# Kernel optimization log

Hardware: AMD Instinct MI355X
Metric: run time of the kernel (lower is better)

## Reference

```python
import jax, jax.numpy as jnp
import numpy as np

COULOMB_CONSTANT = -1.0
EV = 1.602e-19
MAX_ELEMENT = 100
N_ATOMS = 4096
HIDDEN = 16
EMB_ROWS = MAX_ELEMENT * (MAX_ELEMENT + 1) // 2  # 5050


def setup_inputs() -> dict:
    key = jax.random.key(0)
    ks = jax.random.split(key, 8)
    coordinates = jax.random.normal(ks[0], (N_ATOMS, 3), dtype=jnp.float32) * 5.0
    atom_ix = jax.random.randint(ks[1], (N_ATOMS,), 0, MAX_ELEMENT)
    charges = jax.random.normal(ks[2], (N_ATOMS,), dtype=jnp.float32)
    # embedding table [EMB_ROWS, 1]
    emb = jax.random.normal(ks[3], (EMB_ROWS, 1), dtype=jnp.float32)
    # FeedforwardNetwork sizes [2] + [16] + [3]: Linear(2,16), ReLU, Linear(16,3)
    W1 = jax.random.normal(ks[4], (2, HIDDEN), dtype=jnp.float32) / np.sqrt(2.0)
    b1 = jnp.zeros((HIDDEN,), dtype=jnp.float32)
    W2 = jax.random.normal(ks[5], (HIDDEN, 3), dtype=jnp.float32) / np.sqrt(HIDDEN)
    b2 = jnp.zeros((3,), dtype=jnp.float32)
    bias = jax.random.normal(ks[6], (1,), dtype=jnp.float32)
    return {"coordinates": coordinates, "atom_ix": atom_ix, "charges": charges,
            "emb": emb, "W1": W1, "b1": b1, "W2": W2, "b2": b2, "bias": bias}


def reference(coordinates, atom_ix, charges, emb, W1, b1, W2, b2, bias):
    # pairwise distances [N, N]
    diff = coordinates[None, :, :] - coordinates[:, None, :]
    sq = jnp.sum(diff * diff, axis=-1)
    pos = sq > 0
    d_safe = jnp.sqrt(jnp.where(pos, sq, 1.0))
    # torch: nan_to_num(1/d, 0.0) maps diagonal inf -> huge -> clamped to 10
    reciprocal_d = jnp.where(pos, jnp.minimum(1.0 / d_safe, 10.0), 10.0)
    # pairwise embedding gather: index i*(i+1)//2 + j
    pairwise_atom_ix = atom_ix[:, None] * (atom_ix[:, None] + 1) // 2 + atom_ix[None, :]
    pairwise_atom_emb = emb[pairwise_atom_ix, 0]  # [N, N]
    pairwise_charges = charges[:, None] * charges[None, :]  # [N, N]
    model_inputs = jnp.stack([pairwise_atom_emb, pairwise_charges], axis=-1)  # [N, N, 2]
    # tiny MLP: 2 -> 16 -> 3
    h = jax.nn.relu(jnp.einsum('nmi,ih->nmh', model_inputs, W1) + b1)
    atom_weights = jnp.einsum('nmh,ho->nmo', h, W2) + b2  # [N, N, 3]
    c_weights = atom_weights[..., 0]
    lj_sigma = atom_weights[..., 1]
    lj_r = atom_weights[..., 2]
    c_energy = COULOMB_CONSTANT * jnp.sum(c_weights * reciprocal_d)
    sr = lj_sigma * reciprocal_d
    sr6 = sr ** 6
    lj_energy = EV * jnp.sum(lj_r * (sr6 * sr6 - sr6))
    return c_energy + lj_energy + bias
```

## Files before the change

### kernel.cpp

```cpp
#include <hip/hip_runtime.h>
#include <hip/hip_bf16.h>
#include <stdint.h>

#define THREADS 256
#define ROWS_PER_BLOCK 8
#define JSPLIT 4
#define EMB_ROWS 5050

typedef _Float16 half2v __attribute__((ext_vector_type(2)));
typedef __fp16   fp16x2 __attribute__((ext_vector_type(2)));

__device__ __forceinline__ half2v pk(float a, float b) {
    fp16x2 r = __builtin_amdgcn_cvt_pkrtz(a, b);
    return __builtin_bit_cast(half2v, r);
}
__device__ __forceinline__ half2v pkfma(half2v a, half2v b, half2v c) {
    return __builtin_elementwise_fma(a, b, c);
}

__global__ __launch_bounds__(THREADS, 4) void energy_main_kernel(
    const float* __restrict__ coords,
    const int*   __restrict__ atom_ix,
    const float* __restrict__ charges,
    const float* __restrict__ emb,
    const float* __restrict__ W1,
    const float* __restrict__ b1,
    const float* __restrict__ W2,
    const float* __restrict__ b2,
    float* __restrict__ partials,
    int n_atoms)
{
    __shared__ uint32_t s_emb2[EMB_ROWS];
    for (int t = threadIdx.x; t < EMB_ROWS; t += THREADS) {
        const float e = emb[t];
        s_emb2[t] = __builtin_bit_cast(uint32_t, pk(e, e));
    }

    half2v A2[8], B2[8], U0_2[8], U1_2[8], U2_2[8];
    uint32_t C2v[8];
#pragma unroll
    for (int p = 0; p < 8; ++p) {
        A2[p]   = pk(W1[2 * p],      W1[2 * p + 1]);
        B2[p]   = pk(W1[16 + 2 * p], W1[16 + 2 * p + 1]);
        C2v[p]  = __builtin_bit_cast(uint32_t, pk(b1[2 * p], b1[2 * p + 1]));
        asm("" : "+v"(C2v[p]));
        U0_2[p] = pk(W2[3 * (2 * p) + 0], W2[3 * (2 * p + 1) + 0]);
        U1_2[p] = pk(W2[3 * (2 * p) + 1], W2[3 * (2 * p + 1) + 1]);
        U2_2[p] = pk(W2[3 * (2 * p) + 2], W2[3 * (2 * p + 1) + 2]);
    }
    const float bo0 = b2[0], bo1 = b2[1], bo2 = b2[2];

    const int rb   = blockIdx.x / JSPLIT;
    const int js   = blockIdx.x % JSPLIT;
    const int row0 = rb * ROWS_PER_BLOCK;
    const int jlen = n_atoms / JSPLIT;
    const int j0   = js * jlen;

    float  xr[ROWS_PER_BLOCK], yr[ROWS_PER_BLOCK], zr[ROWS_PER_BLOCK];
    half2v qr2[ROWS_PER_BLOCK];
    int    br[ROWS_PER_BLOCK];
#pragma unroll
    for (int r = 0; r < ROWS_PER_BLOCK; ++r) {
        const int i = row0 + r;
        xr[r] = coords[3 * i + 0];
        yr[r] = coords[3 * i + 1];
        zr[r] = coords[3 * i + 2];
        const float q = charges[i];
        qr2[r] = pk(q, q);
        const int a = atom_ix[i];
        br[r] = (a * (a + 1)) >> 1;
    }
    __syncthreads();

    float cacc = 0.0f, ljacc = 0.0f;
    const half2v zero2 = (half2v)(_Float16)0.0f;

#pragma unroll 1
    for (int j = j0 + threadIdx.x; j < j0 + jlen; j += THREADS) {
        const float xj = coords[3 * j + 0];
        const float yj = coords[3 * j + 1];
        const float zj = coords[3 * j + 2];
        const float qj = charges[j];
        const half2v qj2 = pk(qj, qj);
        const int   aj = atom_ix[j];

#pragma unroll
        for (int r = 0; r < ROWS_PER_BLOCK; ++r) {
            const float dx = xj - xr[r];
            const float dy = yj - yr[r];
            const float dz = zj - zr[r];
            const float sq = fmaf(dx, dx, fmaf(dy, dy, dz * dz));
            const float rd = fminf(__builtin_amdgcn_rsqf(sq), 10.0f);

            const half2v e2 = __builtin_bit_cast(half2v, s_emb2[br[r] + aj]);
            const half2v c2 = qr2[r] * qj2;

            float o0 = bo0, o1 = bo1, o2 = bo2;
#pragma unroll
            for (int p = 0; p < 8; ++p) {
                half2v t = pkfma(c2, B2[p], __builtin_bit_cast(half2v, C2v[p]));
                t = pkfma(e2, A2[p], t);
                t = __builtin_elementwise_max(t, zero2);
                o0 = __builtin_amdgcn_fdot2(t, U0_2[p], o0, false);
                o1 = __builtin_amdgcn_fdot2(t, U1_2[p], o1, false);
                o2 = __builtin_amdgcn_fdot2(t, U2_2[p], o2, false);
            }

            cacc = fmaf(o0, rd, cacc);
            const float sr  = o1 * rd;
            const float sr2 = sr * sr;
            const float sr6 = sr2 * sr2 * sr2;
            ljacc = fmaf(o2, fmaf(sr6, sr6, -sr6), ljacc);
        }
    }

#pragma unroll
    for (int off = 32; off > 0; off >>= 1) {
        cacc  += __shfl_down(cacc, off, 64);
        ljacc += __shfl_down(ljacc, off, 64);
    }
    __shared__ float s_c[THREADS / 64], s_l[THREADS / 64];
    const int wave = threadIdx.x >> 6;
    const int lane = threadIdx.x & 63;
    if (lane == 0) { s_c[wave] = cacc; s_l[wave] = ljacc; }
    __syncthreads();
    if (threadIdx.x == 0) {
        float ct = 0.0f, lt = 0.0f;
#pragma unroll
        for (int w = 0; w < THREADS / 64; ++w) { ct += s_c[w]; lt += s_l[w]; }
        partials[2 * blockIdx.x + 0] = ct;
        partials[2 * blockIdx.x + 1] = lt;
    }
}

__global__ __launch_bounds__(THREADS, 1) void energy_reduce_kernel(
    const float* __restrict__ partials, int nblocks,
    const float* __restrict__ bias, float* __restrict__ out)
{
    float ct = 0.0f, lt = 0.0f;
    for (int b = threadIdx.x; b < nblocks; b += THREADS) {
        ct += partials[2 * b + 0];
        lt += partials[2 * b + 1];
    }
#pragma unroll
    for (int off = 32; off > 0; off >>= 1) {
        ct += __shfl_down(ct, off, 64);
        lt += __shfl_down(lt, off, 64);
    }
    __shared__ float s_c[THREADS / 64], s_l[THREADS / 64];
    const int wave = threadIdx.x >> 6;
    const int lane = threadIdx.x & 63;
    if (lane == 0) { s_c[wave] = ct; s_l[wave] = lt; }
    __syncthreads();
    if (threadIdx.x == 0) {
        float c = 0.0f, l = 0.0f;
#pragma unroll
        for (int w = 0; w < THREADS / 64; ++w) { c += s_c[w]; l += s_l[w]; }
        out[0] = -c + 1.602e-19f * l + bias[0];
    }
}

extern "C" void kernel_launch(void* const* d_in, const int* in_sizes, int n_in,
                              void* d_out, int out_size, void* d_ws, size_t ws_size,
                              hipStream_t stream)
{
    const float* coords  = (const float*)d_in[0];
    const int*   atom_ix = (const int*)d_in[1];
    const float* charges = (const float*)d_in[2];
    const float* emb     = (const float*)d_in[3];
    const float* W1      = (const float*)d_in[4];
    const float* b1      = (const float*)d_in[5];
    const float* W2      = (const float*)d_in[6];
    const float* b2      = (const float*)d_in[7];
    const float* bias    = (const float*)d_in[8];

    float* out      = (float*)d_out;
    float* partials = (float*)d_ws;

    const int n       = in_sizes[1];
    const int nblocks = (n / ROWS_PER_BLOCK) * JSPLIT;

    energy_main_kernel<<<nblocks, THREADS, 0, stream>>>(
        coords, atom_ix, charges, emb, W1, b1, W2, b2, partials, n);
    energy_reduce_kernel<<<1, THREADS, 0, stream>>>(partials, nblocks, bias, out);
}
```

Baseline: 43.98 us.

## Pack coords and charges into float4, prefetch next j, uniform weights in SGPRs

Adds a pre-pass kernel that packs coordinates and charges into float4 records in workspace, so each j iteration issues one vector load instead of four scalar ones. The next iteration's atom data is software-prefetched, and MLP weights are forced into scalar registers via readfirstlane to reduce VGPR pressure. JSPLIT is halved to 2, giving fewer blocks that each run longer, and the LDS embedding address is precomputed as a byte offset. The extra kernel launch adds fixed overhead, and the smaller grid may reduce load balance across CUs.

```diff
diff --git a/kernel.cpp b/kernel.cpp
--- a/kernel.cpp
+++ b/kernel.cpp
@@ -4,8 +4,9 @@
 
 #define THREADS 256
 #define ROWS_PER_BLOCK 8
-#define JSPLIT 4
+#define JSPLIT 2
 #define EMB_ROWS 5050
+#define PACK_OFF 65536
 
 typedef _Float16 half2v __attribute__((ext_vector_type(2)));
 typedef __fp16   fp16x2 __attribute__((ext_vector_type(2)));
@@ -17,16 +18,29 @@
 __device__ __forceinline__ half2v pkfma(half2v a, half2v b, half2v c) {
     return __builtin_elementwise_fma(a, b, c);
 }
+__device__ __forceinline__ half2v sgpr(half2v v) {
+    return __builtin_bit_cast(half2v,
+        __builtin_amdgcn_readfirstlane(__builtin_bit_cast(int, v)));
+}
+
+__global__ __launch_bounds__(THREADS) void pack_kernel(
+    const float* __restrict__ coords, const float* __restrict__ charges,
+    float4* __restrict__ pack, int n)
+{
+    const int i = blockIdx.x * THREADS + threadIdx.x;
+    if (i < n)
+        pack[i] = make_float4(coords[3 * i], coords[3 * i + 1],
+                              coords[3 * i + 2], charges[i]);
+}
 
 __global__ __launch_bounds__(THREADS, 4) void energy_main_kernel(
-    const float* __restrict__ coords,
-    const int*   __restrict__ atom_ix,
-    const float* __restrict__ charges,
-    const float* __restrict__ emb,
-    const float* __restrict__ W1,
-    const float* __restrict__ b1,
-    const float* __restrict__ W2,
-    const float* __restrict__ b2,
+    const float4* __restrict__ pack,
+    const int*    __restrict__ atom_ix,
+    const float*  __restrict__ emb,
+    const float*  __restrict__ W1,
+    const float*  __restrict__ b1,
+    const float*  __restrict__ W2,
+    const float*  __restrict__ b2,
     float* __restrict__ partials,
     int n_atoms)
 {
@@ -40,13 +54,13 @@
     uint32_t C2v[8];
 #pragma unroll
     for (int p = 0; p < 8; ++p) {
-        A2[p]   = pk(W1[2 * p],      W1[2 * p + 1]);
-        B2[p]   = pk(W1[16 + 2 * p], W1[16 + 2 * p + 1]);
+        A2[p]   = sgpr(pk(W1[2 * p],      W1[2 * p + 1]));
+        B2[p]   = sgpr(pk(W1[16 + 2 * p], W1[16 + 2 * p + 1]));
         C2v[p]  = __builtin_bit_cast(uint32_t, pk(b1[2 * p], b1[2 * p + 1]));
         asm("" : "+v"(C2v[p]));
-        U0_2[p] = pk(W2[3 * (2 * p) + 0], W2[3 * (2 * p + 1) + 0]);
-        U1_2[p] = pk(W2[3 * (2 * p) + 1], W2[3 * (2 * p + 1) + 1]);
-        U2_2[p] = pk(W2[3 * (2 * p) + 2], W2[3 * (2 * p + 1) + 2]);
+        U0_2[p] = sgpr(pk(W2[3 * (2 * p) + 0], W2[3 * (2 * p + 1) + 0]));
+        U1_2[p] = sgpr(pk(W2[3 * (2 * p) + 1], W2[3 * (2 * p + 1) + 1]));
+        U2_2[p] = sgpr(pk(W2[3 * (2 * p) + 2], W2[3 * (2 * p + 1) + 2]));
     }
     const float bo0 = b2[0], bo1 = b2[1], bo2 = b2[2];
 
@@ -55,44 +69,47 @@
     const int row0 = rb * ROWS_PER_BLOCK;
     const int jlen = n_atoms / JSPLIT;
     const int j0   = js * jlen;
+    const int jend = j0 + jlen;
 
     float  xr[ROWS_PER_BLOCK], yr[ROWS_PER_BLOCK], zr[ROWS_PER_BLOCK];
     half2v qr2[ROWS_PER_BLOCK];
-    int    br[ROWS_PER_BLOCK];
+    int    brb4[ROWS_PER_BLOCK];
 #pragma unroll
     for (int r = 0; r < ROWS_PER_BLOCK; ++r) {
         const int i = row0 + r;
-        xr[r] = coords[3 * i + 0];
-        yr[r] = coords[3 * i + 1];
-        zr[r] = coords[3 * i + 2];
-        const float q = charges[i];
-        qr2[r] = pk(q, q);
+        const float4 p = pack[i];
+        xr[r] = p.x; yr[r] = p.y; zr[r] = p.z;
+        qr2[r] = pk(p.w, p.w);
         const int a = atom_ix[i];
-        br[r] = (a * (a + 1)) >> 1;
+        brb4[r] = ((a * (a + 1)) >> 1) << 2;
     }
     __syncthreads();
 
     float cacc = 0.0f, ljacc = 0.0f;
     const half2v zero2 = (half2v)(_Float16)0.0f;
+    const char* sbase = (const char*)s_emb2;
+
+    float4 pj = pack[j0 + threadIdx.x];
+    int    aj = atom_ix[j0 + threadIdx.x];
 
 #pragma unroll 1
-    for (int j = j0 + threadIdx.x; j < j0 + jlen; j += THREADS) {
-        const float xj = coords[3 * j + 0];
-        const float yj = coords[3 * j + 1];
-        const float zj = coords[3 * j + 2];
-        const float qj = charges[j];
-        const half2v qj2 = pk(qj, qj);
-        const int   aj = atom_ix[j];
+    for (int j = j0 + threadIdx.x; j < jend; j += THREADS) {
+        const int jn = (j + THREADS < jend) ? (j + THREADS) : j;
+        const float4 pn = pack[jn];
+        const int    an = atom_ix[jn];
+
+        const half2v qj2 = pk(pj.w, pj.w);
+        const int    ajb = aj << 2;
 
 #pragma unroll
         for (int r = 0; r < ROWS_PER_BLOCK; ++r) {
-            const float dx = xj - xr[r];
-            const float dy = yj - yr[r];
-            const float dz = zj - zr[r];
+            const float dx = pj.x - xr[r];
+            const float dy = pj.y - yr[r];
+            const float dz = pj.z - zr[r];
             const float sq = fmaf(dx, dx, fmaf(dy, dy, dz * dz));
             const float rd = fminf(__builtin_amdgcn_rsqf(sq), 10.0f);
 
-            const half2v e2 = __builtin_bit_cast(half2v, s_emb2[br[r] + aj]);
+            const half2v e2 = *(const half2v*)(sbase + brb4[r] + ajb);
             const half2v c2 = qr2[r] * qj2;
 
             float o0 = bo0, o1 = bo1, o2 = bo2;
@@ -112,6 +129,8 @@
             const float sr6 = sr2 * sr2 * sr2;
             ljacc = fmaf(o2, fmaf(sr6, sr6, -sr6), ljacc);
         }
+
+        pj = pn; aj = an;
     }
 
 #pragma unroll
@@ -174,13 +193,16 @@
     const float* b2      = (const float*)d_in[7];
     const float* bias    = (const float*)d_in[8];
 
-    float* out      = (float*)d_out;
-    float* partials = (float*)d_ws;
+    float*  out      = (float*)d_out;
+    float*  partials = (float*)d_ws;
+    float4* pack     = (float4*)((char*)d_ws + PACK_OFF);
 
     const int n       = in_sizes[1];
     const int nblocks = (n / ROWS_PER_BLOCK) * JSPLIT;
 
+    pack_kernel<<<(n + THREADS - 1) / THREADS, THREADS, 0, stream>>>(
+        coords, charges, pack, n);
     energy_main_kernel<<<nblocks, THREADS, 0, stream>>>(
-        coords, atom_ix, charges, emb, W1, b1, W2, b2, partials, n);
+        pack, atom_ix, emb, W1, b1, W2, b2, partials, n);
     energy_reduce_kernel<<<1, THREADS, 0, stream>>>(partials, nblocks, bias, out);
 }
```

New measurement: 48.97 us. 11.3% more time.
